# Kernel optimization log

Hardware: AMD Instinct MI355X
Metric: run time of the kernel (lower is better)

The kernel has to match this reference:

```python
import jax, jax.numpy as jnp
import numpy as np

B, S, D = 4, 2048, 1024
H = 16
DH = D // H


def setup_inputs() -> dict:
    key = jax.random.key(0)
    ks = jax.random.split(key, 9)
    s = 0.02
    return {
        "x": jax.random.normal(ks[0], (B, S, D), dtype=jnp.float32),
        "Wq": jax.random.normal(ks[1], (D, D), dtype=jnp.float32) * s,
        "bq": jax.random.normal(ks[2], (D,), dtype=jnp.float32) * s,
        "Wk": jax.random.normal(ks[3], (D, D), dtype=jnp.float32) * s,
        "bk": jax.random.normal(ks[4], (D,), dtype=jnp.float32) * s,
        "Wv": jax.random.normal(ks[5], (D, D), dtype=jnp.float32) * s,
        "bv": jax.random.normal(ks[6], (D,), dtype=jnp.float32) * s,
        "Wo": jax.random.normal(ks[7], (D, D), dtype=jnp.float32) * s,
        "bo": jax.random.normal(ks[8], (D,), dtype=jnp.float32) * s,
    }


def _split_heads(t):
    # [B,S,D] -> [B,H,S,DH]
    b, s, d = t.shape
    return t.reshape(b, s, H, DH).transpose(0, 2, 1, 3)


def reference(x, Wq, bq, Wk, bk, Wv, bv, Wo, bo):
    q = _split_heads(x @ Wq.T + bq)
    k = _split_heads(x @ Wk.T + bk)
    v = _split_heads(x @ Wv.T + bv)
    scale = 1.0 / np.sqrt(DH).astype(np.float32)
    scores = jnp.einsum("bhqd,bhkd->bhqk", q, k) * scale  # [B,H,S,S]
    s = scores.shape[-2]
    causal = jnp.tril(jnp.ones((s, s), dtype=bool))
    scores = jnp.where(causal[None, None], scores, -jnp.inf)
    probs = jax.nn.softmax(scores, axis=-1)
    out = jnp.einsum("bhqk,bhkd->bhqd", probs, v)  # [B,H,S,DH]
    out = out.transpose(0, 2, 1, 3).reshape(x.shape[0], s, D)
    return out @ Wo.T + bo
```

## Files before the change

kernel.cpp:

```cpp
#include <hip/hip_runtime.h>
#include <hip/hip_bf16.h>
#include <cstdint>
#include <cstddef>


typedef unsigned short u16;
typedef __bf16 bf16x8 __attribute__((ext_vector_type(8)));
typedef float  f32x4  __attribute__((ext_vector_type(4)));

__device__ __forceinline__ u16 f2bf(float f) {
  unsigned u = __float_as_uint(f);
  unsigned r = u + 0x7fffu + ((u >> 16) & 1u);
  return (u16)(r >> 16);
}

__device__ __forceinline__ void llds16(const u16* g, u16* l) {
  __builtin_amdgcn_global_load_lds(
      (const __attribute__((address_space(1))) void*)g,
      (__attribute__((address_space(3))) void*)l, 16, 0, 0);
}

__global__ void cast_bf16_kernel(const float* __restrict__ in, u16* __restrict__ out, int n4) {
  int i = blockIdx.x * blockDim.x + threadIdx.x;
  if (i >= n4) return;
  float4 f = ((const float4*)in)[i];
  ushort4 u;
  u.x = f2bf(f.x); u.y = f2bf(f.y); u.z = f2bf(f.z); u.w = f2bf(f.w);
  ((ushort4*)out)[i] = u;
}

__global__ void cast4_kernel(const float* __restrict__ a, const float* __restrict__ b,
                             const float* __restrict__ c, const float* __restrict__ d,
                             u16* __restrict__ oa, u16* __restrict__ ob,
                             u16* __restrict__ oc, u16* __restrict__ od, int n4) {
  const int w = blockIdx.y;
  const float* src = (w == 0) ? a : (w == 1) ? b : (w == 2) ? c : d;
  u16* dst = (w == 0) ? oa : (w == 1) ? ob : (w == 2) ? oc : od;
  int i = blockIdx.x * blockDim.x + threadIdx.x;
  if (i >= n4) return;
  float4 f = ((const float4*)src)[i];
  ushort4 u;
  u.x = f2bf(f.x); u.y = f2bf(f.y); u.z = f2bf(f.z); u.w = f2bf(f.w);
  ((ushort4*)dst)[i] = u;
}

__global__ __launch_bounds__(512, 2) void gemm_qkv_256(
    const u16* __restrict__ A, const u16* __restrict__ Bw,
    const float* __restrict__ b0, const float* __restrict__ b1, const float* __restrict__ b2,
    u16* __restrict__ qkv_out)
{
  __shared__ u16 lds[65536];

  const int tid = threadIdx.x;
  const int lane = tid & 63;
  const int wave = tid >> 6;

  const int bid = (int)blockIdx.x;
  const int c2 = (bid & 7) * 48 + (bid >> 3);
  const int mt = c2 / 12;
  const int nt = c2 - mt * 12;
  const int m0 = mt << 8;
  const int n0 = nt << 8;

  const int warp_m = wave >> 2;
  const int warp_n = wave & 3;
  const int wm = warp_m << 7;
  const int wn = warp_n << 6;
  const int fr = lane & 15;
  const int g  = lane >> 4;

  const int srow = tid >> 3;
  const int schk = ((tid & 7) ^ (srow & 7)) << 3;
  const u16* pA = A  + (size_t)(m0 + srow) * 1024 + schk;
  const u16* pB = Bw + (size_t)(n0 + srow) * 1024 + schk;

  const int rsw0 = ((g    ) ^ (fr & 7)) << 3;
  const int rsw1 = ((g ^ 4) ^ (fr & 7)) << 3;

  const u16* Ab0 = lds + warp_m * 8192 + fr * 64;
  const u16* Bb0 = lds + 16384 + (warp_n >> 1) * 8192 + (warp_n & 1) * 4096 + fr * 64;
  const u16* Ab1 = Ab0 + 32768;
  const u16* Bb1 = Bb0 + 32768;

  f32x4 acc[8][4];
  const f32x4 zero = {0.f, 0.f, 0.f, 0.f};
#pragma unroll
  for (int i = 0; i < 8; i++)
#pragma unroll
    for (int j = 0; j < 4; j++) acc[i][j] = zero;

  bf16x8 a_[4][2];
  bf16x8 b_[4][2];

  auto stage = [&](int kt, int buf, int matBoff, int half, const u16* psrc) {
    const u16* src = psrc + (size_t)half * 131072 + (kt << 6);
    u16* dst = lds + buf * 32768 + matBoff + half * 8192 + tid * 8;
    llds16(src, dst);
    llds16(src + 65536, dst + 4096);
  };
  auto loadA = [&](const u16* Ab, int ib) {
#pragma unroll
    for (int ii = 0; ii < 4; ii++) {
      const u16* r = Ab + (ib + ii) * 1024;
      a_[ii][0] = *(const bf16x8*)(r + rsw0);
      a_[ii][1] = *(const bf16x8*)(r + rsw1);
    }
  };
  auto loadB2 = [&](const u16* Bb, int jb) {
#pragma unroll
    for (int jj = 0; jj < 2; jj++) {
      const u16* r = Bb + (jb + jj) * 1024;
      b_[jb + jj][0] = *(const bf16x8*)(r + rsw0);
      b_[jb + jj][1] = *(const bf16x8*)(r + rsw1);
    }
  };
  auto mfma8 = [&](int ib, int jb) {
    __builtin_amdgcn_s_setprio(1);
#pragma unroll
    for (int jj = 0; jj < 2; jj++)
#pragma unroll
      for (int ii = 0; ii < 4; ii++) {
        acc[ib+ii][jb+jj] = __builtin_amdgcn_mfma_f32_16x16x32_bf16(
            a_[ii][0], b_[jb+jj][0], acc[ib+ii][jb+jj], 0, 0, 0);
        acc[ib+ii][jb+jj] = __builtin_amdgcn_mfma_f32_16x16x32_bf16(
            a_[ii][1], b_[jb+jj][1], acc[ib+ii][jb+jj], 0, 0, 0);
      }
    __builtin_amdgcn_s_setprio(0);
  };

  stage(0, 0, 0,     0, pA);
  stage(0, 0, 0,     1, pA);
  stage(0, 0, 16384, 0, pB);
  stage(0, 0, 16384, 1, pB);
  stage(1, 1, 0,     0, pA);
  asm volatile("s_waitcnt vmcnt(2)" ::: "memory");
  __builtin_amdgcn_s_barrier();

  const int NTI = 8;
  for (int t = 0; t < NTI; ++t) {
    const bool st = (t < NTI - 1);
    const int ka = 2 * t + 1;
    const int kb = 2 * t + 2;
    const int kc = 2 * t + 3;

    loadA(Ab0, 0); loadB2(Bb0, 0);
    stage(ka, 1, 0, 1, pA);
    __builtin_amdgcn_s_barrier();
    mfma8(0, 0);
    __builtin_amdgcn_s_barrier();
    loadB2(Bb0, 2);
    stage(ka, 1, 16384, 0, pB);
    __builtin_amdgcn_s_barrier();
    mfma8(0, 2);
    __builtin_amdgcn_s_barrier();
    loadA(Ab0, 4);
    stage(ka, 1, 16384, 1, pB);
    __builtin_amdgcn_s_barrier();
    mfma8(4, 2);
    __builtin_amdgcn_s_barrier();
    if (st) stage(kb, 0, 0, 0, pA);
    __builtin_amdgcn_s_barrier();
    mfma8(4, 0);
    if (st) { asm volatile("s_waitcnt vmcnt(2)" ::: "memory"); }
    else    { asm volatile("s_waitcnt vmcnt(0)" ::: "memory"); }
    __builtin_amdgcn_s_barrier();

    loadA(Ab1, 0); loadB2(Bb1, 0);
    if (st) stage(kb, 0, 0, 1, pA);
    __builtin_amdgcn_s_barrier();
    mfma8(0, 0);
    __builtin_amdgcn_s_barrier();
    loadB2(Bb1, 2);
    if (st) stage(kb, 0, 16384, 0, pB);
    __builtin_amdgcn_s_barrier();
    mfma8(0, 2);
    __builtin_amdgcn_s_barrier();
    loadA(Ab1, 4);
    if (st) stage(kb, 0, 16384, 1, pB);
    __builtin_amdgcn_s_barrier();
    mfma8(4, 2);
    __builtin_amdgcn_s_barrier();
    if (st) stage(kc, 1, 0, 0, pA);
    __builtin_amdgcn_s_barrier();
    mfma8(4, 0);
    if (st) { asm volatile("s_waitcnt vmcnt(2)" ::: "memory"); }
    __builtin_amdgcn_s_barrier();
  }

  const int rbase = g * 4;
  const int which = n0 >> 10;
  const float* bias = (which == 0) ? b0 : ((which == 1) ? b1 : b2);
  const float post = (which == 0) ? 0.18033688011f : 1.0f;
  u16* outb = qkv_out + (size_t)which * 8388608;
#pragma unroll
  for (int j = 0; j < 4; j++) {
    const int nn = (n0 + wn + j * 16 + fr) & 1023;
    const float bb = bias[nn];
    const int h = nn >> 6, dh = nn & 63;
#pragma unroll
    for (int i = 0; i < 8; i++) {
#pragma unroll
      for (int r = 0; r < 4; r++) {
        const int m = m0 + wm + i * 16 + rbase + r;
        const int bI = m >> 11, s = m & 2047;
        outb[(((size_t)bI * 16 + h) * 2048 + s) * 64 + dh] = f2bf((acc[i][j][r] + bb) * post);
      }
    }
  }
}

__global__ __launch_bounds__(256) void gemm_bt(
    const u16* __restrict__ A, const u16* __restrict__ Bw,
    const float* __restrict__ b0, const float* __restrict__ b1, const float* __restrict__ b2,
    u16* __restrict__ qkv_out, float* __restrict__ flat_out,
    int K, int mode)
{
  __shared__ u16 As[128 * 32];
  __shared__ u16 Bs[128 * 32];

  const int tid = threadIdx.x;
  const int n0 = blockIdx.x * 128;
  const int m0 = blockIdx.y * 128;

  const int srow = tid >> 2;
  const int soff = (tid & 3) * 8;
  const u16* gA0 = A  + (size_t)(m0 + srow) * K + soff;
  const u16* gA1 = gA0 + (size_t)64 * K;
  const u16* gB0 = Bw + (size_t)(n0 + srow) * K + soff;
  const u16* gB1 = gB0 + (size_t)64 * K;
  u16* lA0 = As + tid * 8;
  u16* lA1 = As + 2048 + tid * 8;
  u16* lB0 = Bs + tid * 8;
  u16* lB1 = Bs + 2048 + tid * 8;

  const int lane = tid & 63;
  const int wave = tid >> 6;
  const int wm = (wave >> 1) * 64;
  const int wn = (wave & 1) * 64;
  const int fr = lane & 15;
  const int k8 = (lane >> 4) * 8;

  f32x4 zero = {0.f, 0.f, 0.f, 0.f};
  f32x4 acc[4][4];
#pragma unroll
  for (int i = 0; i < 4; i++)
#pragma unroll
    for (int j = 0; j < 4; j++) acc[i][j] = zero;

  for (int k0 = 0; k0 < K; k0 += 32) {
    llds16(gA0 + k0, lA0);
    llds16(gA1 + k0, lA1);
    llds16(gB0 + k0, lB0);
    llds16(gB1 + k0, lB1);
    __syncthreads();
    bf16x8 af[4], bfr[4];
#pragma unroll
    for (int i = 0; i < 4; i++)
      af[i] = *(const bf16x8*)(As + (wm + i * 16 + fr) * 32 + k8);
#pragma unroll
    for (int j = 0; j < 4; j++)
      bfr[j] = *(const bf16x8*)(Bs + (wn + j * 16 + fr) * 32 + k8);
#pragma unroll
    for (int i = 0; i < 4; i++)
#pragma unroll
      for (int j = 0; j < 4; j++)
        acc[i][j] = __builtin_amdgcn_mfma_f32_16x16x32_bf16(af[i], bfr[j], acc[i][j], 0, 0, 0);
    __syncthreads();
  }

  const int rbase = (lane >> 4) * 4;
  if (mode == 0) {
    const int which = n0 >> 10;
    const float* bias = (which == 0) ? b0 : ((which == 1) ? b1 : b2);
    const float post = (which == 0) ? 0.18033688011f : 1.0f;
    u16* outb = qkv_out + (size_t)which * 8388608;
#pragma unroll
    for (int j = 0; j < 4; j++) {
      const int nn = (n0 + wn + j * 16 + fr) & 1023;
      const float bb = bias[nn];
      const int h = nn >> 6, dh = nn & 63;
#pragma unroll
      for (int i = 0; i < 4; i++) {
#pragma unroll
        for (int r = 0; r < 4; r++) {
          const int m = m0 + wm + i * 16 + rbase + r;
          const int bI = m >> 11, s = m & 2047;
          outb[(((size_t)bI * 16 + h) * 2048 + s) * 64 + dh] = f2bf((acc[i][j][r] + bb) * post);
        }
      }
    }
  } else {
#pragma unroll
    for (int j = 0; j < 4; j++) {
      const int n = n0 + wn + j * 16 + fr;
      const float bb = b0[n];
#pragma unroll
      for (int i = 0; i < 4; i++) {
#pragma unroll
        for (int r = 0; r < 4; r++) {
          const int m = m0 + wm + i * 16 + rbase + r;
          flat_out[(size_t)m * 1024 + n] = acc[i][j][r] + bb;
        }
      }
    }
  }
}

__global__ __launch_bounds__(256) void transpose_v(const u16* __restrict__ V, u16* __restrict__ VT) {
  __shared__ u16 t_s[64 * 72];
  const int tid = threadIdx.x;
  const int st = blockIdx.x << 6;
  const int bh = blockIdx.y;
  const u16* src = V + ((size_t)bh * 2048 + st) * 64;
#pragma unroll
  for (int p = 0; p < 2; p++) {
    int i = p * 256 + tid;
    int row = i >> 3, ch = i & 7;
    bf16x8 v = *(const bf16x8*)(src + row * 64 + ch * 8);
    *(bf16x8*)(t_s + row * 72 + ch * 8) = v;
  }
  __syncthreads();
  u16* dst = VT + (size_t)bh * 131072 + st;
#pragma unroll
  for (int p = 0; p < 2; p++) {
    int i = p * 256 + tid;
    int dh = i >> 3, ch = i & 7;
    union { u16 s[8]; bf16x8 v; } u;
#pragma unroll
    for (int e = 0; e < 8; e++) u.s[e] = t_s[(ch * 8 + e) * 72 + dh];
    *(bf16x8*)(dst + (size_t)dh * 2048 + ch * 8) = u.v;
  }
}

__global__ __launch_bounds__(256, 2) void attn_fa(
    const u16* __restrict__ Qb, const u16* __restrict__ Kb,
    const u16* __restrict__ VT, u16* __restrict__ Ob)
{
  __shared__ u16 k_s[2 * 4096];
  __shared__ u16 v_s[2 * 4096];
  __shared__ u16 p_s[2 * 9216];
  __shared__ float l_s[256];

  const int tid = threadIdx.x;
  const int lane = tid & 63;
  const int wave = tid >> 6;

  const int c = (int)blockIdx.x;
  const int xcd = c & 7;
  const int rr_ = c >> 3;
  const int bh = xcd + ((rr_ >> 3) << 3);
  const int pr = rr_ & 7;
  const int qtA = pr;
  const int qtB = 15 - pr;

  const size_t head = (size_t)bh << 17;
  const int fr = lane & 15;
  const int g = lane >> 4;
  const int k8 = g << 3;
  const int q0A = qtA << 7;
  const int q0B = qtB << 7;
  const int wrow = wave << 5;

  bf16x8 aqA[2][2], aqB[2][2];
#pragma unroll
  for (int f = 0; f < 2; f++) {
    const u16* qpA = Qb + head + (size_t)(q0A + wrow + (f << 4) + fr) * 64;
    aqA[f][0] = *(const bf16x8*)(qpA + k8);
    aqA[f][1] = *(const bf16x8*)(qpA + 32 + k8);
    const u16* qpB = Qb + head + (size_t)(q0B + wrow + (f << 4) + fr) * 64;
    aqB[f][0] = *(const bf16x8*)(qpB + k8);
    aqB[f][1] = *(const bf16x8*)(qpB + 32 + k8);
  }

  const int r0 = tid >> 3, c0 = tid & 7;
  const int r1 = 32 + r0;
  const int koff0 = r0 * 64 + (((c0 ^ r0) & 7) << 3);
  const int koff1 = r1 * 64 + (((c0 ^ r1) & 7) << 3);
  const int voff0 = r0 * 2048 + (((c0 ^ r0) & 7) << 3);
  const int voff1 = r1 * 2048 + (((c0 ^ r1) & 7) << 3);
  int kaddr[4][2], vaddr[2][4];
#pragma unroll
  for (int j = 0; j < 4; j++) {
    const int kn = (j << 4) + fr;
    kaddr[j][0] = kn * 64 + (((g ^ kn) & 7) << 3);
    kaddr[j][1] = kn * 64 + ((((g + 4) ^ kn) & 7) << 3);
#pragma unroll
    for (int s2 = 0; s2 < 2; s2++)
      vaddr[s2][j] = kn * 64 + ((((s2 << 2) + g) ^ (kn & 7)) << 3);
  }
  u16* const prowA0 = p_s + (wrow + fr) * 72;
  u16* const prowA1 = p_s + (wrow + 16 + fr) * 72;
  u16* const prowB0 = p_s + 9216 + (wrow + fr) * 72;
  u16* const prowB1 = p_s + 9216 + (wrow + 16 + fr) * 72;
  const u16* Kbase = Kb + head;
  const u16* Vbase = VT + head;

  auto issueK = [&](int jt2, int buf) {
    const u16* Kt = Kbase + ((size_t)jt2 << 12);
    llds16(Kt + koff0, k_s + (buf << 12) + tid * 8);
    llds16(Kt + koff1, k_s + (buf << 12) + 2048 + tid * 8);
  };
  auto issueV = [&](int jt2, int buf) {
    const u16* Vt = Vbase + (jt2 << 6);
    llds16(Vt + voff0, v_s + (buf << 12) + tid * 8);
    llds16(Vt + voff1, v_s + (buf << 12) + 2048 + tid * 8);
  };

  f32x4 oA[2][4], oB[2][4];
  const f32x4 zero = {0.f, 0.f, 0.f, 0.f};
#pragma unroll
  for (int f = 0; f < 2; f++)
#pragma unroll
    for (int j = 0; j < 4; j++) { oA[f][j] = zero; oB[f][j] = zero; }
  float lA[2] = {0.f, 0.f}, lB[2] = {0.f, 0.f};

  const int jmax = 2 * qtB + 1;
  const int diagA = 2 * qtA + (wave >> 1);
  const int diagB = 2 * qtB + (wave >> 1);

  auto do_pv = [&](const u16* vs, f32x4 (&oacc)[2][4], const u16* p0r, const u16* p1r) {
#pragma unroll
    for (int s2 = 0; s2 < 2; s2++) {
      const bf16x8 ap0 = *(const bf16x8*)(p0r + (s2 << 5) + k8);
      const bf16x8 ap1 = *(const bf16x8*)(p1r + (s2 << 5) + k8);
#pragma unroll
      for (int j = 0; j < 4; j++) {
        const bf16x8 bv = *(const bf16x8*)(vs + vaddr[s2][j]);
        oacc[0][j] = __builtin_amdgcn_mfma_f32_16x16x32_bf16(ap0, bv, oacc[0][j], 0, 0, 0);
        oacc[1][j] = __builtin_amdgcn_mfma_f32_16x16x32_bf16(ap1, bv, oacc[1][j], 0, 0, 0);
      }
    }
  };

  auto do_s = [&](const u16* ks, int jt, bool dodiag, int q0t,
                  const bf16x8 (&aqt)[2][2], float (&lr)[2], u16* p0r, u16* p1r) {
    f32x4 s_acc[2][4];
#pragma unroll
    for (int f = 0; f < 2; f++)
#pragma unroll
      for (int j = 0; j < 4; j++) s_acc[f][j] = zero;
#pragma unroll
    for (int j = 0; j < 4; j++) {
      const bf16x8 ka0 = *(const bf16x8*)(ks + kaddr[j][0]);
      const bf16x8 ka1 = *(const bf16x8*)(ks + kaddr[j][1]);
      s_acc[0][j] = __builtin_amdgcn_mfma_f32_16x16x32_bf16(ka0, aqt[0][0], s_acc[0][j], 0, 0, 0);
      s_acc[0][j] = __builtin_amdgcn_mfma_f32_16x16x32_bf16(ka1, aqt[0][1], s_acc[0][j], 0, 0, 0);
      s_acc[1][j] = __builtin_amdgcn_mfma_f32_16x16x32_bf16(ka0, aqt[1][0], s_acc[1][j], 0, 0, 0);
      s_acc[1][j] = __builtin_amdgcn_mfma_f32_16x16x32_bf16(ka1, aqt[1][1], s_acc[1][j], 0, 0, 0);
    }
#pragma unroll
    for (int f = 0; f < 2; f++) {
      const int qa = q0t + wrow + (f << 4) + fr;
      u16* prow = (f == 0) ? p0r : p1r;
      if (dodiag) {
#pragma unroll
        for (int j = 0; j < 4; j++) {
          const int ka = (jt << 6) + (j << 4) + (g << 2);
          float p0 = (ka + 0 > qa) ? 0.f : __builtin_amdgcn_exp2f(s_acc[f][j][0]);
          float p1 = (ka + 1 > qa) ? 0.f : __builtin_amdgcn_exp2f(s_acc[f][j][1]);
          float p2 = (ka + 2 > qa) ? 0.f : __builtin_amdgcn_exp2f(s_acc[f][j][2]);
          float p3 = (ka + 3 > qa) ? 0.f : __builtin_amdgcn_exp2f(s_acc[f][j][3]);
          lr[f] += (p0 + p1) + (p2 + p3);
          union { __hip_bfloat162 h; unsigned u; } ca, cb;
          ca.h = __float22bfloat162_rn(make_float2(p0, p1));
          cb.h = __float22bfloat162_rn(make_float2(p2, p3));
          *(uint2*)(prow + (j << 4) + (g << 2)) = make_uint2(ca.u, cb.u);
        }
      } else {
#pragma unroll
        for (int j = 0; j < 4; j++) {
          float p0 = __builtin_amdgcn_exp2f(s_acc[f][j][0]);
          float p1 = __builtin_amdgcn_exp2f(s_acc[f][j][1]);
          float p2 = __builtin_amdgcn_exp2f(s_acc[f][j][2]);
          float p3 = __builtin_amdgcn_exp2f(s_acc[f][j][3]);
          lr[f] += (p0 + p1) + (p2 + p3);
          union { __hip_bfloat162 h; unsigned u; } ca, cb;
          ca.h = __float22bfloat162_rn(make_float2(p0, p1));
          cb.h = __float22bfloat162_rn(make_float2(p2, p3));
          *(uint2*)(prow + (j << 4) + (g << 2)) = make_uint2(ca.u, cb.u);
        }
      }
    }
  };

  issueK(0, 0);

  for (int jt = 0; jt <= jmax; jt++) {
    const int buf = jt & 1;
    __syncthreads();
    if (jt < jmax) issueK(jt + 1, buf ^ 1);
    issueV(jt, buf);
    if (jt > 0) {
      const u16* vprev = v_s + ((buf ^ 1) << 12);
      if (jt - 1 <= diagB) do_pv(vprev, oB, prowB0, prowB1);
      if (jt - 1 <= diagA) do_pv(vprev, oA, prowA0, prowA1);
    }
    if (jt <= diagB) do_s(k_s + (buf << 12), jt, jt == diagB, q0B, aqB, lB, prowB0, prowB1);
    if (jt <= diagA) do_s(k_s + (buf << 12), jt, jt == diagA, q0A, aqA, lA, prowA0, prowA1);
  }
  __syncthreads();
  if (diagB == jmax) do_pv(v_s + ((jmax & 1) << 12), oB, prowB0, prowB1);

#pragma unroll
  for (int f = 0; f < 2; f++) {
    float la = lA[f];
    la += __shfl_xor(la, 16);
    la += __shfl_xor(la, 32);
    if (g == 0) l_s[wrow + (f << 4) + fr] = la;
    float lb = lB[f];
    lb += __shfl_xor(lb, 16);
    lb += __shfl_xor(lb, 32);
    if (g == 0) l_s[128 + wrow + (f << 4) + fr] = lb;
  }
  const int b = bh >> 4, h = bh & 15;
#pragma unroll
  for (int f = 0; f < 2; f++) {
#pragma unroll
    for (int r = 0; r < 4; r++) {
      const int qloc = wrow + (f << 4) + (g << 2) + r;
      const float invA = 1.f / l_s[qloc];
      const float invB = 1.f / l_s[128 + qloc];
      const int qA_abs = q0A + qloc;
      const int qB_abs = q0B + qloc;
#pragma unroll
      for (int j = 0; j < 4; j++) {
        Ob[((size_t)b * 2048 + qA_abs) * 1024 + (h << 6) + (j << 4) + fr] =
            f2bf(oA[f][j][r] * invA);
        Ob[((size_t)b * 2048 + qB_abs) * 1024 + (h << 6) + (j << 4) + fr] =
            f2bf(oB[f][j][r] * invB);
      }
    }
  }
}

extern "C" void kernel_launch(void* const* d_in, const int* in_sizes, int n_in,
                              void* d_out, int out_size, void* d_ws, size_t ws_size,
                              hipStream_t stream) {
  const float* x  = (const float*)d_in[0];
  const float* Wq = (const float*)d_in[1];
  const float* bq = (const float*)d_in[2];
  const float* Wk = (const float*)d_in[3];
  const float* bk = (const float*)d_in[4];
  const float* Wv = (const float*)d_in[5];
  const float* bv = (const float*)d_in[6];
  const float* Wo = (const float*)d_in[7];
  const float* bo = (const float*)d_in[8];
  float* out = (float*)d_out;

  char* ws = (char*)d_ws;
  u16* xb    = (u16*)(ws);
  u16* vT    = (u16*)(ws);
  u16* wqkv  = (u16*)(ws + 16777216);
  u16* wo    = (u16*)(ws + 23068672);
  u16* qkv   = (u16*)(ws + 25165824);
  u16* attnb = (u16*)(ws + 75497472);

  cast_bf16_kernel<<<8192, 256, 0, stream>>>(x, xb, 2097152);
  cast4_kernel<<<dim3(1024, 4), 256, 0, stream>>>(
      Wq, Wk, Wv, Wo, wqkv, wqkv + 1048576, wqkv + 2097152, wo, 262144);

  gemm_qkv_256<<<dim3(384), 512, 0, stream>>>(xb, wqkv, bq, bk, bv, qkv);

  transpose_v<<<dim3(32, 64), 256, 0, stream>>>(qkv + 16777216, vT);

  attn_fa<<<dim3(512), 256, 0, stream>>>(qkv, qkv + 8388608, vT, attnb);

  gemm_bt<<<dim3(8, 64), 256, 0, stream>>>(attnb, wo, bo, bo, bo, nullptr, out, 1024, 1);
}
```

Baseline: 269.2 us.

## Retile QKV GEMM to 256x192 tiles and stage epilogue through LDS

The QKV projection GEMM moves from 256x256 tiles (384 blocks) to 256x192 tiles (512 blocks), so the grid fills all CUs evenly across the 8 XCDs, and the block-to-tile mapping is rewritten for the new layout. The LDS footprint and accumulator count shrink, and launch_bounds no longer requests 2 blocks per CU. The epilogue now writes biased, scaled bf16 results into LDS and then stores 16-byte vectors to the head-split layout, replacing scattered 2-byte global stores. The risks are lower MFMA work per tile loaded, an uneven B staging pattern, and an extra LDS round trip plus barriers in the epilogue.

```diff
diff --git a/kernel.cpp b/kernel.cpp
--- a/kernel.cpp
+++ b/kernel.cpp
@@ -44,28 +44,29 @@
   ((ushort4*)dst)[i] = u;
 }
 
-__global__ __launch_bounds__(512, 2) void gemm_qkv_256(
+__global__ __launch_bounds__(512) void gemm_qkv_256(
     const u16* __restrict__ A, const u16* __restrict__ Bw,
     const float* __restrict__ b0, const float* __restrict__ b1, const float* __restrict__ b2,
     u16* __restrict__ qkv_out)
 {
-  __shared__ u16 lds[65536];
+  __shared__ u16 lds[57344];
 
   const int tid = threadIdx.x;
   const int lane = tid & 63;
   const int wave = tid >> 6;
 
   const int bid = (int)blockIdx.x;
-  const int c2 = (bid & 7) * 48 + (bid >> 3);
-  const int mt = c2 / 12;
-  const int nt = c2 - mt * 12;
+  const int xcd = bid & 7;
+  const int idx = bid >> 3;
+  const int mt = (xcd << 2) | (idx & 3);
+  const int nt = idx >> 2;
   const int m0 = mt << 8;
-  const int n0 = nt << 8;
+  const int n0 = nt * 192;
 
   const int warp_m = wave >> 2;
   const int warp_n = wave & 3;
   const int wm = warp_m << 7;
-  const int wn = warp_n << 6;
+  const int wn = warp_n * 48;
   const int fr = lane & 15;
   const int g  = lane >> 4;
 
@@ -77,28 +78,39 @@
   const int rsw0 = ((g    ) ^ (fr & 7)) << 3;
   const int rsw1 = ((g ^ 4) ^ (fr & 7)) << 3;
 
-  const u16* Ab0 = lds + warp_m * 8192 + fr * 64;
-  const u16* Bb0 = lds + 16384 + (warp_n >> 1) * 8192 + (warp_n & 1) * 4096 + fr * 64;
-  const u16* Ab1 = Ab0 + 32768;
-  const u16* Bb1 = Bb0 + 32768;
-
-  f32x4 acc[8][4];
+  const u16* Ab0 = lds + (size_t)(wm + fr) * 64;
+  const u16* Bb0 = lds + 16384 + (size_t)(wn + fr) * 64;
+  const u16* Ab1 = Ab0 + 28672;
+  const u16* Bb1 = Bb0 + 28672;
+
+  f32x4 acc[8][3];
   const f32x4 zero = {0.f, 0.f, 0.f, 0.f};
 #pragma unroll
   for (int i = 0; i < 8; i++)
 #pragma unroll
-    for (int j = 0; j < 4; j++) acc[i][j] = zero;
+    for (int j = 0; j < 3; j++) acc[i][j] = zero;
 
   bf16x8 a_[4][2];
-  bf16x8 b_[4][2];
-
-  auto stage = [&](int kt, int buf, int matBoff, int half, const u16* psrc) {
-    const u16* src = psrc + (size_t)half * 131072 + (kt << 6);
-    u16* dst = lds + buf * 32768 + matBoff + half * 8192 + tid * 8;
+  bf16x8 b_[3][2];
+
+  auto stageA = [&](int kt, int buf, int half) {
+    const u16* src = pA + (size_t)half * 131072 + (kt << 6);
+    u16* dst = lds + buf * 28672 + half * 8192 + tid * 8;
     llds16(src, dst);
     llds16(src + 65536, dst + 4096);
   };
-  auto loadA = [&](const u16* Ab, int ib) {
+  auto stageB0 = [&](int kt, int buf) {
+    const u16* src = pB + (kt << 6);
+    u16* dst = lds + buf * 28672 + 16384 + tid * 8;
+    llds16(src, dst);
+    llds16(src + 65536, dst + 4096);
+  };
+  auto stageB1 = [&](int kt, int buf) {
+    const u16* src = pB + 131072 + (kt << 6);
+    u16* dst = lds + buf * 28672 + 24576 + tid * 8;
+    llds16(src, dst);
+  };
+  auto loadA4 = [&](const u16* Ab, int ib) {
 #pragma unroll
     for (int ii = 0; ii < 4; ii++) {
       const u16* r = Ab + (ib + ii) * 1024;
@@ -106,33 +118,38 @@
       a_[ii][1] = *(const bf16x8*)(r + rsw1);
     }
   };
-  auto loadB2 = [&](const u16* Bb, int jb) {
-#pragma unroll
-    for (int jj = 0; jj < 2; jj++) {
-      const u16* r = Bb + (jb + jj) * 1024;
-      b_[jb + jj][0] = *(const bf16x8*)(r + rsw0);
-      b_[jb + jj][1] = *(const bf16x8*)(r + rsw1);
-    }
-  };
-  auto mfma8 = [&](int ib, int jb) {
+  auto loadB = [&](const u16* Bb, int j0, int nj) {
+#pragma unroll
+    for (int jj = 0; jj < 3; jj++) {
+      if (jj < nj) {
+        const u16* r = Bb + (j0 + jj) * 1024;
+        b_[j0 + jj][0] = *(const bf16x8*)(r + rsw0);
+        b_[j0 + jj][1] = *(const bf16x8*)(r + rsw1);
+      }
+    }
+  };
+  auto mfmaQ = [&](int ib, int j0, int nj) {
     __builtin_amdgcn_s_setprio(1);
 #pragma unroll
-    for (int jj = 0; jj < 2; jj++)
-#pragma unroll
-      for (int ii = 0; ii < 4; ii++) {
-        acc[ib+ii][jb+jj] = __builtin_amdgcn_mfma_f32_16x16x32_bf16(
-            a_[ii][0], b_[jb+jj][0], acc[ib+ii][jb+jj], 0, 0, 0);
-        acc[ib+ii][jb+jj] = __builtin_amdgcn_mfma_f32_16x16x32_bf16(
-            a_[ii][1], b_[jb+jj][1], acc[ib+ii][jb+jj], 0, 0, 0);
-      }
+    for (int jj = 0; jj < 3; jj++) {
+      if (jj < nj) {
+#pragma unroll
+        for (int ii = 0; ii < 4; ii++) {
+          acc[ib+ii][j0+jj] = __builtin_amdgcn_mfma_f32_16x16x32_bf16(
+              a_[ii][0], b_[j0+jj][0], acc[ib+ii][j0+jj], 0, 0, 0);
+          acc[ib+ii][j0+jj] = __builtin_amdgcn_mfma_f32_16x16x32_bf16(
+              a_[ii][1], b_[j0+jj][1], acc[ib+ii][j0+jj], 0, 0, 0);
+        }
+      }
+    }
     __builtin_amdgcn_s_setprio(0);
   };
 
-  stage(0, 0, 0,     0, pA);
-  stage(0, 0, 0,     1, pA);
-  stage(0, 0, 16384, 0, pB);
-  stage(0, 0, 16384, 1, pB);
-  stage(1, 1, 0,     0, pA);
+  stageA(0, 0, 0);
+  stageA(0, 0, 1);
+  stageB0(0, 0);
+  stageB1(0, 0);
+  stageA(1, 1, 0);
   asm volatile("s_waitcnt vmcnt(2)" ::: "memory");
   __builtin_amdgcn_s_barrier();
 
@@ -143,69 +160,81 @@
     const int kb = 2 * t + 2;
     const int kc = 2 * t + 3;
 
-    loadA(Ab0, 0); loadB2(Bb0, 0);
-    stage(ka, 1, 0, 1, pA);
-    __builtin_amdgcn_s_barrier();
-    mfma8(0, 0);
-    __builtin_amdgcn_s_barrier();
-    loadB2(Bb0, 2);
-    stage(ka, 1, 16384, 0, pB);
-    __builtin_amdgcn_s_barrier();
-    mfma8(0, 2);
-    __builtin_amdgcn_s_barrier();
-    loadA(Ab0, 4);
-    stage(ka, 1, 16384, 1, pB);
-    __builtin_amdgcn_s_barrier();
-    mfma8(4, 2);
-    __builtin_amdgcn_s_barrier();
-    if (st) stage(kb, 0, 0, 0, pA);
-    __builtin_amdgcn_s_barrier();
-    mfma8(4, 0);
+    loadA4(Ab0, 0); loadB(Bb0, 0, 2);
+    stageA(ka, 1, 1);
+    __builtin_amdgcn_s_barrier();
+    mfmaQ(0, 0, 2);
+    __builtin_amdgcn_s_barrier();
+    loadB(Bb0, 2, 1);
+    stageB0(ka, 1);
+    __builtin_amdgcn_s_barrier();
+    mfmaQ(0, 2, 1);
+    __builtin_amdgcn_s_barrier();
+    loadA4(Ab0, 4);
+    stageB1(ka, 1);
+    __builtin_amdgcn_s_barrier();
+    mfmaQ(4, 2, 1);
+    __builtin_amdgcn_s_barrier();
+    if (st) stageA(kb, 0, 0);
+    __builtin_amdgcn_s_barrier();
+    mfmaQ(4, 0, 2);
     if (st) { asm volatile("s_waitcnt vmcnt(2)" ::: "memory"); }
     else    { asm volatile("s_waitcnt vmcnt(0)" ::: "memory"); }
     __builtin_amdgcn_s_barrier();
 
-    loadA(Ab1, 0); loadB2(Bb1, 0);
-    if (st) stage(kb, 0, 0, 1, pA);
-    __builtin_amdgcn_s_barrier();
-    mfma8(0, 0);
-    __builtin_amdgcn_s_barrier();
-    loadB2(Bb1, 2);
-    if (st) stage(kb, 0, 16384, 0, pB);
-    __builtin_amdgcn_s_barrier();
-    mfma8(0, 2);
-    __builtin_amdgcn_s_barrier();
-    loadA(Ab1, 4);
-    if (st) stage(kb, 0, 16384, 1, pB);
-    __builtin_amdgcn_s_barrier();
-    mfma8(4, 2);
-    __builtin_amdgcn_s_barrier();
-    if (st) stage(kc, 1, 0, 0, pA);
-    __builtin_amdgcn_s_barrier();
-    mfma8(4, 0);
+    loadA4(Ab1, 0); loadB(Bb1, 0, 2);
+    if (st) stageA(kb, 0, 1);
+    __builtin_amdgcn_s_barrier();
+    mfmaQ(0, 0, 2);
+    __builtin_amdgcn_s_barrier();
+    loadB(Bb1, 2, 1);
+    if (st) stageB0(kb, 0);
+    __builtin_amdgcn_s_barrier();
+    mfmaQ(0, 2, 1);
+    __builtin_amdgcn_s_barrier();
+    loadA4(Ab1, 4);
+    if (st) stageB1(kb, 0);
+    __builtin_amdgcn_s_barrier();
+    mfmaQ(4, 2, 1);
+    __builtin_amdgcn_s_barrier();
+    if (st) stageA(kc, 1, 0);
+    __builtin_amdgcn_s_barrier();
+    mfmaQ(4, 0, 2);
     if (st) { asm volatile("s_waitcnt vmcnt(2)" ::: "memory"); }
     __builtin_amdgcn_s_barrier();
   }
 
-  const int rbase = g * 4;
-  const int which = n0 >> 10;
-  const float* bias = (which == 0) ? b0 : ((which == 1) ? b1 : b2);
-  const float post = (which == 0) ? 0.18033688011f : 1.0f;
-  u16* outb = qkv_out + (size_t)which * 8388608;
-#pragma unroll
-  for (int j = 0; j < 4; j++) {
-    const int nn = (n0 + wn + j * 16 + fr) & 1023;
-    const float bb = bias[nn];
-    const int h = nn >> 6, dh = nn & 63;
+  __syncthreads();
+  const int bI  = m0 >> 11;
+  const int s0m = m0 & 2047;
+#pragma unroll
+  for (int j = 0; j < 3; j++) {
+    const int ncol = n0 + wn + j * 16 + fr;
+    const int which = ncol >> 10;
+    const float bb = ((which == 0) ? b0 : (which == 1) ? b1 : b2)[ncol & 1023];
+    const float post = (which == 0) ? 0.18033688011f : 1.0f;
+    const int cl = wn + j * 16 + fr;
 #pragma unroll
     for (int i = 0; i < 8; i++) {
 #pragma unroll
       for (int r = 0; r < 4; r++) {
-        const int m = m0 + wm + i * 16 + rbase + r;
-        const int bI = m >> 11, s = m & 2047;
-        outb[(((size_t)bI * 16 + h) * 2048 + s) * 64 + dh] = f2bf((acc[i][j][r] + bb) * post);
-      }
-    }
+        const int row = wm + i * 16 + g * 4 + r;
+        lds[row * 200 + cl] = f2bf((acc[i][j][r] + bb) * post);
+      }
+    }
+  }
+  __syncthreads();
+  const int part = tid & 7;
+#pragma unroll
+  for (int p = 0; p < 12; p++) {
+    const int hc = p >> 2;
+    const int ml = ((p & 3) << 6) + (tid >> 3);
+    const int ncol0 = n0 + hc * 64;
+    const int which = ncol0 >> 10;
+    const int h = (ncol0 >> 6) & 15;
+    const bf16x8 v = *(const bf16x8*)(lds + ml * 200 + hc * 64 + part * 8);
+    *(bf16x8*)(qkv_out + (size_t)which * 8388608 +
+               ((size_t)(bI * 16 + h) * 2048 + s0m + ml) * 64 + part * 8) = v;
   }
 }
 
@@ -559,7 +588,7 @@
   cast4_kernel<<<dim3(1024, 4), 256, 0, stream>>>(
       Wq, Wk, Wv, Wo, wqkv, wqkv + 1048576, wqkv + 2097152, wo, 262144);
 
-  gemm_qkv_256<<<dim3(384), 512, 0, stream>>>(xb, wqkv, bq, bk, bv, qkv);
+  gemm_qkv_256<<<dim3(512), 512, 0, stream>>>(xb, wqkv, bq, bk, bv, qkv);
 
   transpose_v<<<dim3(32, 64), 256, 0, stream>>>(qkv + 16777216, vT);
 
```

Result: faster. 256.3 us (-4.8%).
